# Optimization experiments

Hardware: AMD Instinct MI355X
Metric: run time of the kernel (lower is better)

The kernel has to match this reference:

```python
import jax, jax.numpy as jnp
import numpy as np

WINDOW = 512
N_GLOBAL = 32


def setup_inputs() -> dict:
    key = jax.random.key(0)
    kq, kk, kv = jax.random.split(key, 3)
    shape = (2, 16, 8192, 64)  # [batch, heads, seq_len, head_dim]
    q = jax.random.normal(kq, shape, dtype=jnp.float32)
    k = jax.random.normal(kk, shape, dtype=jnp.float32)
    v = jax.random.normal(kv, shape, dtype=jnp.float32)
    return {"q": q, "k": k, "v": v}


def _sliding_window_attention(q, k, v):
    # Faithful to the torch loop: for i in range(0, S, W) the window is
    # [max(0, i-W//2), min(S, i+W//2)). For S a multiple of W these windows are
    # contiguous, non-overlapping chunks: chunk0 = [0, W//2), then (n-1) chunks
    # of width W. Concatenated output covers positions [0, S - W//2).
    B, H, S, D = q.shape
    W, G, half = WINDOW, N_GLOBAL, WINDOW // 2
    n = S // W
    scale = 1.0 / (D ** 0.5)

    kg = k[:, :, :G]  # [B,H,G,D] global keys
    vg = v[:, :, :G]

    # --- first chunk: positions [0, half) ---
    q0 = q[:, :, :half]
    kc0 = jnp.concatenate([kg, k[:, :, :half]], axis=2)  # [B,H,G+half,D]
    vc0 = jnp.concatenate([vg, v[:, :, :half]], axis=2)
    s0 = jnp.einsum('bhqd,bhkd->bhqk', q0, kc0) * scale
    o0 = jnp.einsum('bhqk,bhkd->bhqd', jax.nn.softmax(s0, axis=-1), vc0)

    # --- remaining (n-1) chunks of width W: positions [half, S-half) ---
    C = n - 1
    qr = q[:, :, half:S - half].reshape(B, H, C, W, D)
    kr = k[:, :, half:S - half].reshape(B, H, C, W, D)
    vr = v[:, :, half:S - half].reshape(B, H, C, W, D)
    kgb = jnp.broadcast_to(kg[:, :, None], (B, H, C, G, D))
    vgb = jnp.broadcast_to(vg[:, :, None], (B, H, C, G, D))
    kc = jnp.concatenate([kgb, kr], axis=3)  # [B,H,C,G+W,D]
    vc = jnp.concatenate([vgb, vr], axis=3)
    s = jnp.einsum('bhcqd,bhckd->bhcqk', qr, kc) * scale
    o = jnp.einsum('bhcqk,bhckd->bhcqd', jax.nn.softmax(s, axis=-1), vc)
    o = o.reshape(B, H, C * W, D)

    return jnp.concatenate([o0, o], axis=2)  # [B,H,S - W//2,D]


def reference(q, k, v):
    return _sliding_window_attention(q, k, v)
```

## Files before the change

kernel.cpp:

```cpp
#include <hip/hip_runtime.h>
#include <hip/hip_bf16.h>

typedef __bf16 v8bf16 __attribute__((ext_vector_type(8)));
typedef __bf16 v2bf16 __attribute__((ext_vector_type(2)));
typedef float  v4f    __attribute__((ext_vector_type(4)));
typedef unsigned int u32;

#define SEQ     8192
#define DIM     64
#define OUTSEQ  7936
#define WIN     512
#define HALF    256
#define BH      32
#define NCHUNK  15
#define MAXT    17
#define NWG_CH  1920
#define VROW    584

__device__ __forceinline__ v8bf16 cvt8(v4f a, v4f b) {
    v8bf16 r;
    r[0] = (__bf16)a[0]; r[1] = (__bf16)a[1];
    r[2] = (__bf16)a[2]; r[3] = (__bf16)a[3];
    r[4] = (__bf16)b[0]; r[5] = (__bf16)b[1];
    r[6] = (__bf16)b[2]; r[7] = (__bf16)b[3];
    return r;
}

__device__ __forceinline__ v8bf16 load8bf(const float* __restrict__ p) {
    const v4f a = *(const v4f*)p;
    const v4f b = *(const v4f*)(p + 4);
    return cvt8(a, b);
}

__device__ __forceinline__ u32 pk2(float lo, float hi) {
    v2bf16 p; p[0] = (__bf16)lo; p[1] = (__bf16)hi;
    return __builtin_bit_cast(u32, p);
}

__device__ __forceinline__ int vt_idx(int d, int col) {
    return d * VROW + (col ^ (((d >> 3) & 7) << 3));
}

__global__ __launch_bounds__(256, 2)
void swa_fwd(const float* __restrict__ qg,
             const float* __restrict__ kg,
             const float* __restrict__ vg,
             float* __restrict__ outg)
{
    __shared__ __align__(16) __bf16 Vt[DIM * VROW];

    const int b = blockIdx.x;
    int bh, qoff, koff, ntiles;
    if (b < NWG_CH) {
        const int x  = b & 7;
        const int j  = b >> 3;
        const int qt = j & 3;
        const int cg = ((j >> 2) << 3) | x;
        bh = cg / NCHUNK;
        const int c = cg - bh * NCHUNK;
        koff = HALF + c * WIN;
        qoff = koff + qt * 128;
        ntiles = MAXT;
    } else {
        const int i = b - NWG_CH;
        bh = i >> 1;
        qoff = (i & 1) * 128;
        koff = 0;
        ntiles = 9;
    }

    const float* qb = qg + (size_t)bh * SEQ * DIM;
    const float* kb = kg + (size_t)bh * SEQ * DIM;
    const float* vb = vg + (size_t)bh * SEQ * DIM;

    const int tid  = threadIdx.x;
    const int wave = tid >> 6;
    const int lane = tid & 63;
    const int l15  = lane & 15;
    const int quad = lane >> 4;

    const int qbase = qoff + wave * 32;
    v8bf16 qf[2][2];
    #pragma unroll
    for (int qs = 0; qs < 2; ++qs) {
        const float* qp = qb + (size_t)(qbase + qs * 16 + l15) * DIM + quad * 8;
        qf[qs][0] = load8bf(qp);
        qf[qs][1] = load8bf(qp + 32);
    }

    {
        const int keyduo = tid >> 4;
        const int dquad  = tid & 15;
        #pragma unroll 4
        for (int t = 0; t < ntiles; ++t) {
            const int base = (t == 0) ? 0 : koff + (t - 1) * 32;
            const int tokA = base + 2 * keyduo;
            const v4f a  = *(const v4f*)(vb + (size_t)tokA * DIM + dquad * 4);
            const v4f b2 = *(const v4f*)(vb + (size_t)(tokA + 1) * DIM + dquad * 4);
            const int colA = t * 32 + 2 * keyduo;
            #pragma unroll
            for (int i = 0; i < 4; ++i) {
                v2bf16 pr; pr[0] = (__bf16)a[i]; pr[1] = (__bf16)b2[i];
                *(v2bf16*)(&Vt[vt_idx(dquad * 4 + i, colA)]) = pr;
            }
        }
    }
    __syncthreads();

    const float cexp = 0.125f * 1.44269504089f;
    const v4f vzero = {0.f, 0.f, 0.f, 0.f};
    float lsum[2] = {0.f, 0.f};
    v4f oacc[2][4];
    #pragma unroll
    for (int qs = 0; qs < 2; ++qs)
        #pragma unroll
        for (int dt = 0; dt < 4; ++dt) oacc[qs][dt] = vzero;

    const int srcA = ((quad & 1) << 5) + l15;
    const int srcB = srcA + 16;
    const bool hi  = quad >= 2;

    #pragma unroll 2
    for (int t = 0; t < ntiles; ++t) {
        const int base = (t == 0) ? 0 : koff + (t - 1) * 32;
        const int tcol = t * 32;

        const float* kp = kb + (size_t)(base + l15) * DIM + quad * 8;
        const v8bf16 k00 = load8bf(kp);
        const v8bf16 k01 = load8bf(kp + 32);
        const v8bf16 k10 = load8bf(kp + 16 * DIM);
        const v8bf16 k11 = load8bf(kp + 16 * DIM + 32);

        v8bf16 vf[4];
        #pragma unroll
        for (int dt = 0; dt < 4; ++dt)
            vf[dt] = *(const v8bf16*)(&Vt[vt_idx(dt * 16 + l15, tcol + quad * 8)]);

        #pragma unroll
        for (int qs = 0; qs < 2; ++qs) {
            const v4f S0 = __builtin_amdgcn_mfma_f32_16x16x32_bf16(k01, qf[qs][1],
                           __builtin_amdgcn_mfma_f32_16x16x32_bf16(k00, qf[qs][0], vzero, 0,0,0), 0,0,0);
            const v4f S1 = __builtin_amdgcn_mfma_f32_16x16x32_bf16(k11, qf[qs][1],
                           __builtin_amdgcn_mfma_f32_16x16x32_bf16(k10, qf[qs][0], vzero, 0,0,0), 0,0,0);

            float e0[4], e1[4];
            #pragma unroll
            for (int rr = 0; rr < 4; ++rr) {
                e0[rr] = __builtin_exp2f(S0[rr] * cexp);
                e1[rr] = __builtin_exp2f(S1[rr] * cexp);
                lsum[qs] += e0[rr] + e1[rr];
            }
            const u32 A0 = pk2(e0[0], e0[1]), B0 = pk2(e0[2], e0[3]);
            const u32 A1 = pk2(e1[0], e1[1]), B1 = pk2(e1[2], e1[3]);

            const u32 t0 = (u32)__shfl((int)A0, srcA, 64), u0 = (u32)__shfl((int)A1, srcA, 64);
            const u32 t1 = (u32)__shfl((int)B0, srcA, 64), u1 = (u32)__shfl((int)B1, srcA, 64);
            const u32 t2 = (u32)__shfl((int)A0, srcB, 64), u2 = (u32)__shfl((int)A1, srcB, 64);
            const u32 t3 = (u32)__shfl((int)B0, srcB, 64), u3 = (u32)__shfl((int)B1, srcB, 64);
            u32 pd[4];
            pd[0] = hi ? u0 : t0;  pd[1] = hi ? u1 : t1;
            pd[2] = hi ? u2 : t2;  pd[3] = hi ? u3 : t3;
            const v8bf16 pf = __builtin_bit_cast(v8bf16, *(const u32(*)[4])pd);

            #pragma unroll
            for (int dt = 0; dt < 4; ++dt)
                oacc[qs][dt] = __builtin_amdgcn_mfma_f32_16x16x32_bf16(vf[dt], pf, oacc[qs][dt], 0,0,0);
        }
    }

    #pragma unroll
    for (int qs = 0; qs < 2; ++qs) {
        float l = lsum[qs];
        l += __shfl_xor(l, 16, 64);
        l += __shfl_xor(l, 32, 64);
        const float inv = 1.0f / l;
        float* ob = outg + ((size_t)bh * OUTSEQ + qbase + qs * 16 + l15) * DIM;
        #pragma unroll
        for (int dt = 0; dt < 4; ++dt) {
            v4f rv = oacc[qs][dt];
            rv[0] *= inv; rv[1] *= inv; rv[2] *= inv; rv[3] *= inv;
            *(v4f*)(ob + dt * 16 + quad * 4) = rv;
        }
    }
}

extern "C" void kernel_launch(void* const* d_in, const int* in_sizes, int n_in,
                              void* d_out, int out_size, void* d_ws, size_t ws_size,
                              hipStream_t stream) {
    const float* q = (const float*)d_in[0];
    const float* k = (const float*)d_in[1];
    const float* v = (const float*)d_in[2];
    float* out = (float*)d_out;

    const int n_wg = NWG_CH + BH * 2;
    swa_fwd<<<dim3(n_wg), dim3(256), 0, stream>>>(q, k, v, out);
}
```

Before: 310.7 us.

## Double-buffer transposed V tiles in LDS and raise occupancy to four blocks

Before, the kernel staged the whole window of V (up to 17 tiles) into one large LDS buffer ahead of compute. Now it keeps two 32-key tiles and prefetches the next tile's V into registers while the current tile is computed. The prefetched tile is written into the alternate buffer, followed by a barrier each iteration. This shrinks LDS use sharply so launch bounds can request four blocks per CU, and it overlaps V loading with MFMA work. The cost is a __syncthreads per tile and the loss of the loop unroll.

```diff
diff --git a/kernel.cpp b/kernel.cpp
--- a/kernel.cpp
+++ b/kernel.cpp
@@ -15,7 +15,7 @@
 #define NCHUNK  15
 #define MAXT    17
 #define NWG_CH  1920
-#define VROW    584
+#define VROWT   40
 
 __device__ __forceinline__ v8bf16 cvt8(v4f a, v4f b) {
     v8bf16 r;
@@ -38,16 +38,16 @@
 }
 
 __device__ __forceinline__ int vt_idx(int d, int col) {
-    return d * VROW + (col ^ (((d >> 3) & 7) << 3));
-}
-
-__global__ __launch_bounds__(256, 2)
+    return d * VROWT + (col ^ (((d >> 3) & 3) << 3));
+}
+
+__global__ __launch_bounds__(256, 4)
 void swa_fwd(const float* __restrict__ qg,
              const float* __restrict__ kg,
              const float* __restrict__ vg,
              float* __restrict__ outg)
 {
-    __shared__ __align__(16) __bf16 Vt[DIM * VROW];
+    __shared__ __align__(16) __bf16 Vt[2][DIM * VROWT];
 
     const int b = blockIdx.x;
     int bh, qoff, koff, ntiles;
@@ -88,21 +88,17 @@
         qf[qs][1] = load8bf(qp + 32);
     }
 
+    const int keyduo = tid >> 4;
+    const int dquad  = tid & 15;
+
     {
-        const int keyduo = tid >> 4;
-        const int dquad  = tid & 15;
-        #pragma unroll 4
-        for (int t = 0; t < ntiles; ++t) {
-            const int base = (t == 0) ? 0 : koff + (t - 1) * 32;
-            const int tokA = base + 2 * keyduo;
-            const v4f a  = *(const v4f*)(vb + (size_t)tokA * DIM + dquad * 4);
-            const v4f b2 = *(const v4f*)(vb + (size_t)(tokA + 1) * DIM + dquad * 4);
-            const int colA = t * 32 + 2 * keyduo;
-            #pragma unroll
-            for (int i = 0; i < 4; ++i) {
-                v2bf16 pr; pr[0] = (__bf16)a[i]; pr[1] = (__bf16)b2[i];
-                *(v2bf16*)(&Vt[vt_idx(dquad * 4 + i, colA)]) = pr;
-            }
+        const int tokA = 2 * keyduo;
+        const v4f a  = *(const v4f*)(vb + (size_t)tokA * DIM + dquad * 4);
+        const v4f b2 = *(const v4f*)(vb + (size_t)(tokA + 1) * DIM + dquad * 4);
+        #pragma unroll
+        for (int i = 0; i < 4; ++i) {
+            v2bf16 pr; pr[0] = (__bf16)a[i]; pr[1] = (__bf16)b2[i];
+            *(v2bf16*)(&Vt[0][vt_idx(dquad * 4 + i, 2 * keyduo)]) = pr;
         }
     }
     __syncthreads();
@@ -120,10 +116,17 @@
     const int srcB = srcA + 16;
     const bool hi  = quad >= 2;
 
-    #pragma unroll 2
+    int cur = 0;
     for (int t = 0; t < ntiles; ++t) {
         const int base = (t == 0) ? 0 : koff + (t - 1) * 32;
-        const int tcol = t * 32;
+        const bool have_next = (t + 1 < ntiles);
+
+        v4f sva, svb;
+        if (have_next) {
+            const int tokA = koff + t * 32 + 2 * keyduo;
+            sva = *(const v4f*)(vb + (size_t)tokA * DIM + dquad * 4);
+            svb = *(const v4f*)(vb + (size_t)(tokA + 1) * DIM + dquad * 4);
+        }
 
         const float* kp = kb + (size_t)(base + l15) * DIM + quad * 8;
         const v8bf16 k00 = load8bf(kp);
@@ -131,10 +134,11 @@
         const v8bf16 k10 = load8bf(kp + 16 * DIM);
         const v8bf16 k11 = load8bf(kp + 16 * DIM + 32);
 
+        const __bf16* vcur = Vt[cur];
         v8bf16 vf[4];
         #pragma unroll
         for (int dt = 0; dt < 4; ++dt)
-            vf[dt] = *(const v8bf16*)(&Vt[vt_idx(dt * 16 + l15, tcol + quad * 8)]);
+            vf[dt] = *(const v8bf16*)(&vcur[vt_idx(dt * 16 + l15, quad * 8)]);
 
         #pragma unroll
         for (int qs = 0; qs < 2; ++qs) {
@@ -166,6 +170,17 @@
             for (int dt = 0; dt < 4; ++dt)
                 oacc[qs][dt] = __builtin_amdgcn_mfma_f32_16x16x32_bf16(vf[dt], pf, oacc[qs][dt], 0,0,0);
         }
+
+        if (have_next) {
+            __bf16* vnxt = Vt[cur ^ 1];
+            #pragma unroll
+            for (int i = 0; i < 4; ++i) {
+                v2bf16 pr; pr[0] = (__bf16)sva[i]; pr[1] = (__bf16)svb[i];
+                *(v2bf16*)(&vnxt[vt_idx(dquad * 4 + i, 2 * keyduo)]) = pr;
+            }
+        }
+        __syncthreads();
+        cur ^= 1;
     }
 
     #pragma unroll
```

Result: faster. 297.2 us (-4.3%).
